# Kernel optimization log

Measured on AMD Instinct MI355X. Metric: run time of the kernel, lower is better.

## Reference

```python
import jax, jax.numpy as jnp
import numpy as np

N = 4096    # channels * n = 4 * 1024
N_IN = 1024
FC = 512


def ldr_layer(x, G, H, subd_A, subd_B, bias):
    """y = W x + bias, where W = sum_i K(A, g_i) K(B, h_i)^T and A, B are
    subdiagonal matrices with entries subd_A, subd_B (Krylov LDR fast multiply).

    Closed form: K(A, g)[i, j] = g[i-j] * c[i] / c[i-j] for i >= j (0 otherwise),
    with c = [1, cumprod(subd_A)]. This turns the multiply into FFT
    correlations/convolutions of length 2n instead of a dense n x n GEMM.
    x: (b, n); G, H: (r, n); subd_A, subd_B: (n-1,); bias: (n,).
    """
    n = x.shape[-1]
    one = jnp.ones((1,), x.dtype)
    c = jnp.concatenate([one, jnp.cumprod(subd_A)])   # (n,) cumulative subdiag products of A
    d = jnp.concatenate([one, jnp.cumprod(subd_B)])   # (n,)
    L = 2 * n
    q = H / d                                          # (r, n)
    gp = G / c                                         # (r, n)
    p = x * d                                          # (b, n)
    # u[b, r, j] = (K(B, h_r)^T x)[j] = sum_k q[r, k] * p[b, j + k]  (cross-correlation)
    Fp = jnp.fft.rfft(p, n=L)                          # (b, n+1)
    Fq = jnp.fft.rfft(q, n=L)                          # (r, n+1)
    u = jnp.fft.irfft(Fp[:, None] * jnp.conj(Fq)[None], n=L)[..., :n]  # (b, r, n)
    # out[b, i] = c[i] * sum_r (gp_r * u[b, r])_conv[i]  (causal convolution)
    Fg = jnp.fft.rfft(gp, n=L)                         # (r, n+1)
    Fu = jnp.fft.rfft(u, n=L)                          # (b, r, n+1)
    out = jnp.fft.irfft(jnp.einsum('rk,brk->bk', Fg, Fu), n=L)[:, :n]
    return c * out + bias


def setup_inputs() -> dict:
    key = jax.random.key(0)
    ks = jax.random.split(key, 14)
    std = 0.01  # params.init_stddev
    f32 = jnp.float32
    inp = {
        'x': jax.random.normal(ks[0], (128, N_IN), f32),
        'G1': std * jax.random.normal(ks[1], (48, N), f32),
        'H1': std * jax.random.normal(ks[2], (48, N), f32),
        'subd_A1': jnp.exp(0.01 * jax.random.normal(ks[3], (N - 1,), f32)),
        'subd_B1': jnp.exp(0.01 * jax.random.normal(ks[4], (N - 1,), f32)),
        'b1': std * jax.random.normal(ks[5], (N,), f32),
        'G2': std * jax.random.normal(ks[6], (16, N), f32),
        'H2': std * jax.random.normal(ks[7], (16, N), f32),
        'subd_A2': jnp.exp(0.01 * jax.random.normal(ks[8], (N - 1,), f32)),
        'subd_B2': jnp.exp(0.01 * jax.random.normal(ks[9], (N - 1,), f32)),
        'b2': std * jax.random.normal(ks[10], (N,), f32),
        'W_logits': jax.random.normal(ks[11], (10, FC), f32) / np.sqrt(FC).astype(np.float32),
        'b_logits': std * jax.random.normal(ks[12], (10,), f32),
    }
    return inp


def reference(x, G1, H1, subd_A1, subd_B1, b1, G2, H2, subd_A2, subd_B2, b2,
              W_logits, b_logits):
    bsz, n_in = x.shape
    xp = jnp.concatenate([x, jnp.zeros((bsz, N - n_in), x.dtype)], axis=-1)  # pad to channels*n
    h = jax.nn.relu(ldr_layer(xp, G1, H1, subd_A1, subd_B1, b1))
    h = jax.nn.relu(ldr_layer(h, G2, H2, subd_A2, subd_B2, b2))
    return h[:, :FC] @ W_logits.T + b_logits
```

## Files before the change

### kernel.cpp

```cpp
#include <hip/hip_runtime.h>
#include <hip/hip_bf16.h>

#define BATCH 128
#define NIN   1024
#define NFULL 4096
#define R1    48
#define R2    16
#define FCDIM 512
#define NOUT  10

#define WS_C1  0
#define WS_D1  4096
#define WS_C2  8192
#define WS_D2  12288
#define WS_Q1  16384
#define WS_GP1 (WS_Q1 + R1*NFULL)
#define WS_Q2  (WS_GP1 + R1*NFULL)
#define WS_GP2 (WS_Q2 + R2*NFULL)
#define WS_P1  (WS_GP2 + R2*NFULL)
#define WS_P2  (WS_P1 + BATCH*NIN)
#define WS_H2  (WS_P2 + BATCH*NFULL)
#define WS_PT1 (WS_H2 + BATCH*FCDIM)
#define WS_P2M (WS_PT1 + NIN*NFULL)
#define WS_CT1 (WS_P2M + FCDIM*NFULL)
#define WS_CT2 (WS_CT1 + 8*5120)
#define WS_VP1 (WS_CT2 + 8*4608)
#define WS_VP2 (WS_VP1 + 4*BATCH*NFULL)
#define WS_END (WS_VP2 + 32*BATCH*FCDIM)

#define NCH 8
#define CH1 (NIN / NCH)
#define CH2 (FCDIM / NCH)
#define CTLD1 5120
#define CTLD2 4608

__global__ void __launch_bounds__(256) prep_fused(
    const float* __restrict__ x, const float* __restrict__ G1,
    const float* __restrict__ H1, const float* __restrict__ G2,
    const float* __restrict__ H2, const float* __restrict__ sA1,
    const float* __restrict__ sB1, const float* __restrict__ sA2,
    const float* __restrict__ sB2, float* __restrict__ ws) {
    __shared__ float cd[4096];
    __shared__ float tot[256];
    int b = blockIdx.x, t = threadIdx.x;
    const float* src;
    int kind, r;
    if (b < 48)       { kind = 0; r = b;       src = sB1; }
    else if (b < 96)  { kind = 1; r = b - 48;  src = sA1; }
    else if (b < 112) { kind = 2; r = b - 96;  src = sB2; }
    else if (b < 128) { kind = 3; r = b - 112; src = sA2; }
    else              { kind = 4; r = b - 128; src = sB1; }
    float loc[16];
    float prod = 1.f;
#pragma unroll
    for (int u = 0; u < 16; ++u) {
        int idx = t * 16 + u;
        float e = (idx == 0) ? 1.f : src[idx - 1];
        prod *= e;
        loc[u] = prod;
    }
    tot[t] = prod;
    __syncthreads();
    for (int off = 1; off < 256; off <<= 1) {
        float v = (t >= off) ? tot[t - off] : 1.f;
        __syncthreads();
        tot[t] *= v;
        __syncthreads();
    }
    float excl = (t == 0) ? 1.f : tot[t - 1];
#pragma unroll
    for (int u = 0; u < 16; ++u) cd[t * 16 + u] = excl * loc[u];
    __syncthreads();

    if (kind == 0) {
        const float* s0 = H1 + (size_t)r * NFULL;
        float* dst = ws + WS_Q1 + (size_t)r * NFULL;
#pragma unroll
        for (int u = 0; u < 16; ++u) { int i = t + u * 256; dst[i] = s0[i] / cd[i]; }
        if (r == 0) { float* d1 = ws + WS_D1;
#pragma unroll
            for (int u = 0; u < 16; ++u) { int i = t + u * 256; d1[i] = cd[i]; } }
    } else if (kind == 1) {
        const float* s0 = G1 + (size_t)r * NFULL;
        float* dst = ws + WS_GP1 + (size_t)r * NFULL;
#pragma unroll
        for (int u = 0; u < 16; ++u) { int i = t + u * 256; dst[i] = s0[i] / cd[i]; }
        if (r == 0) { float* c1 = ws + WS_C1;
#pragma unroll
            for (int u = 0; u < 16; ++u) { int i = t + u * 256; c1[i] = cd[i]; } }
    } else if (kind == 2) {
        const float* s0 = H2 + (size_t)r * NFULL;
        float* dst = ws + WS_Q2 + (size_t)r * NFULL;
#pragma unroll
        for (int u = 0; u < 16; ++u) { int i = t + u * 256; dst[i] = s0[i] / cd[i]; }
        if (r == 0) { float* d2 = ws + WS_D2;
#pragma unroll
            for (int u = 0; u < 16; ++u) { int i = t + u * 256; d2[i] = cd[i]; } }
    } else if (kind == 3) {
        const float* s0 = G2 + (size_t)r * NFULL;
        float* dst = ws + WS_GP2 + (size_t)r * NFULL;
#pragma unroll
        for (int u = 0; u < 16; ++u) { int i = t + u * 256; dst[i] = s0[i] / cd[i]; }
        if (r == 0) { float* c2 = ws + WS_C2;
#pragma unroll
            for (int u = 0; u < 16; ++u) { int i = t + u * 256; c2[i] = cd[i]; } }
    } else {
        int row0 = r * 4;
#pragma unroll
        for (int u = 0; u < 16; ++u) {
            int lin = t + u * 256;
            int row = row0 + (lin >> 10), col = lin & 1023;
            ws[WS_P1 + (size_t)row * NIN + col] = x[(size_t)row * NIN + col] * cd[col];
        }
    }
}

__global__ void gemm_rank_kernel(const float* __restrict__ A, const float* __restrict__ B,
                                 float* __restrict__ C, int Mo, int No, int Kr, int ld) {
    __shared__ float As[48 * 64];
    __shared__ float Bs[48 * 64];
    int tid = threadIdx.x;
    int tx = tid & 15, ty = tid >> 4;
    int n0 = blockIdx.x * 64;
    int m0 = blockIdx.y * 64;
    int tot = Kr * 64;
    for (int lin = tid; lin < tot; lin += 256) {
        int r = lin >> 6, i = lin & 63;
        As[lin] = A[r * ld + m0 + i];
        Bs[lin] = B[r * ld + n0 + i];
    }
    __syncthreads();
    float acc[4][4] = {};
    for (int r = 0; r < Kr; ++r) {
        float a4[4], b4[4];
#pragma unroll
        for (int i = 0; i < 4; ++i) a4[i] = As[r * 64 + ty * 4 + i];
#pragma unroll
        for (int j = 0; j < 4; ++j) b4[j] = Bs[r * 64 + tx * 4 + j];
#pragma unroll
        for (int i = 0; i < 4; ++i)
#pragma unroll
            for (int j = 0; j < 4; ++j) acc[i][j] += a4[i] * b4[j];
    }
#pragma unroll
    for (int i = 0; i < 4; ++i) {
        int m = m0 + ty * 4 + i;
#pragma unroll
        for (int j = 0; j < 4; ++j) {
            C[(size_t)m * No + n0 + tx * 4 + j] = acc[i][j];
        }
    }
}

__global__ void diag_scan_p1(float* __restrict__ ws) {
    const int which = blockIdx.z;
    float* P        = ws + (which == 0 ? WS_PT1 : WS_P2M);
    float* ctot     = ws + (which == 0 ? WS_CT1 : WS_CT2);
    const int R     = which == 0 ? NIN : FCDIM;
    const int CH    = which == 0 ? CH1 : CH2;
    const int nd    = R + NFULL - 1;
    const int ctld  = which == 0 ? CTLD1 : CTLD2;
    int t = blockIdx.x * 256 + threadIdx.x;
    if (t >= nd) return;
    int doff = t - (R - 1);
    int z = blockIdx.y;
    int m0 = z * CH;
    int mlo = max(m0, -doff);
    int mhi = min(m0 + CH, min(NFULL - doff, R));
    float run = 0.f;
    if (mlo < mhi) {
        float* p = P + (size_t)mlo * NFULL + (mlo + doff);
        const size_t step = NFULL + 1;
        int len = mhi - mlo;
        int s = 0;
        for (; s + 8 <= len; s += 8) {
            float v[8];
#pragma unroll
            for (int u = 0; u < 8; ++u) v[u] = p[u * step];
#pragma unroll
            for (int u = 0; u < 8; ++u) { run += v[u]; v[u] = run; }
#pragma unroll
            for (int u = 0; u < 8; ++u) p[u * step] = v[u];
            p += 8 * step;
        }
        for (; s < len; ++s) { float v = *p; run += v; *p = run; p += step; }
    }
    ctot[(size_t)z * ctld + t] = run;
}

__global__ void off_prefix(float* __restrict__ ws) {
    const int which = blockIdx.z;
    float* ct      = ws + (which == 0 ? WS_CT1 : WS_CT2);
    const int ctld = which == 0 ? CTLD1 : CTLD2;
    int t = blockIdx.x * 256 + threadIdx.x;
    if (t >= ctld) return;
    float run = 0.f;
#pragma unroll
    for (int z = 0; z < NCH; ++z) {
        float v = ct[(size_t)z * ctld + t];
        ct[(size_t)z * ctld + t] = run;
        run += v;
    }
}

__global__ void __launch_bounds__(512)
gemm2_l1_kernel(const float* __restrict__ p1, const float* __restrict__ Mt1,
                const float* __restrict__ OFF1, float* __restrict__ vp) {
    __shared__ float As[2][32][68];
    __shared__ float Bs[2][32][68];
    int tid = threadIdx.x;
    int g = tid >> 8;
    int t = tid & 255;
    int tx = t & 15, ty = t >> 4;
    int n0 = blockIdx.x * 64;
    int m0 = blockIdx.y * 64;
    int kbase = blockIdx.z * 256 + g * 128;
    const float* offrow = OFF1 + (size_t)(kbase >> 7) * CTLD1;
    float acc[4][4] = {};
    for (int k0 = kbase; k0 < kbase + 128; k0 += 32) {
#pragma unroll
        for (int l = 0; l < 2; ++l) {
            int lin = t + l * 256;
            int m = lin >> 3, k4 = lin & 7;
            float4 v = *(const float4*)&p1[(size_t)(m0 + m) * NIN + k0 + k4 * 4];
            As[g][k4 * 4 + 0][m] = v.x;
            As[g][k4 * 4 + 1][m] = v.y;
            As[g][k4 * 4 + 2][m] = v.z;
            As[g][k4 * 4 + 3][m] = v.w;
        }
#pragma unroll
        for (int l = 0; l < 2; ++l) {
            int lin = t + l * 256;
            int k = lin >> 4, n4 = lin & 15;
            float4 v = *(const float4*)&Mt1[(size_t)(k0 + k) * NFULL + n0 + n4 * 4];
            const float* o = &offrow[1023 + n0 + n4 * 4 - (k0 + k)];
            v.x += o[0]; v.y += o[1]; v.z += o[2]; v.w += o[3];
            *(float4*)&Bs[g][k][n4 * 4] = v;
        }
        __syncthreads();
#pragma unroll
        for (int kk = 0; kk < 32; ++kk) {
            float4 a4 = *(const float4*)&As[g][kk][ty * 4];
            float4 b4 = *(const float4*)&Bs[g][kk][tx * 4];
            acc[0][0] += a4.x * b4.x; acc[0][1] += a4.x * b4.y;
            acc[0][2] += a4.x * b4.z; acc[0][3] += a4.x * b4.w;
            acc[1][0] += a4.y * b4.x; acc[1][1] += a4.y * b4.y;
            acc[1][2] += a4.y * b4.z; acc[1][3] += a4.y * b4.w;
            acc[2][0] += a4.z * b4.x; acc[2][1] += a4.z * b4.y;
            acc[2][2] += a4.z * b4.z; acc[2][3] += a4.z * b4.w;
            acc[3][0] += a4.w * b4.x; acc[3][1] += a4.w * b4.y;
            acc[3][2] += a4.w * b4.z; acc[3][3] += a4.w * b4.w;
        }
        __syncthreads();
    }
    float* red = &As[0][0][0];
    if (g == 1) {
#pragma unroll
        for (int i = 0; i < 4; ++i)
            *(float4*)&red[(ty * 4 + i) * 64 + tx * 4] =
                make_float4(acc[i][0], acc[i][1], acc[i][2], acc[i][3]);
    }
    __syncthreads();
    if (g == 0) {
        float* dst = vp + (size_t)blockIdx.z * BATCH * NFULL;
#pragma unroll
        for (int i = 0; i < 4; ++i) {
            int m = m0 + ty * 4 + i;
            float4 r = *(const float4*)&red[(ty * 4 + i) * 64 + tx * 4];
            *(float4*)&dst[(size_t)m * NFULL + n0 + tx * 4] =
                make_float4(acc[i][0] + r.x, acc[i][1] + r.y,
                            acc[i][2] + r.z, acc[i][3] + r.w);
        }
    }
}

__global__ void reduce_l1_kernel(const float* __restrict__ vp, const float* __restrict__ c1,
                                 const float* __restrict__ b1, const float* __restrict__ d2,
                                 float* __restrict__ p2) {
    int idx4 = blockIdx.x * 256 + threadIdx.x;
    int base = idx4 * 4;
    int n = base & (NFULL - 1);
    float4 s = make_float4(0.f, 0.f, 0.f, 0.f);
#pragma unroll
    for (int z = 0; z < 4; ++z) {
        float4 v = *(const float4*)&vp[(size_t)z * BATCH * NFULL + base];
        s.x += v.x; s.y += v.y; s.z += v.z; s.w += v.w;
    }
    float4 cc = *(const float4*)&c1[n];
    float4 bb = *(const float4*)&b1[n];
    float4 dd = *(const float4*)&d2[n];
    float4 o;
    o.x = fmaxf(cc.x * s.x + bb.x, 0.f) * dd.x;
    o.y = fmaxf(cc.y * s.y + bb.y, 0.f) * dd.y;
    o.z = fmaxf(cc.z * s.z + bb.z, 0.f) * dd.z;
    o.w = fmaxf(cc.w * s.w + bb.w, 0.f) * dd.w;
    *(float4*)&p2[base] = o;
}

__global__ void gemm2_l2_kernel(const float* __restrict__ p2, const float* __restrict__ M2,
                                const float* __restrict__ OFF2, float* __restrict__ vp) {
    __shared__ float As[32][68];
    __shared__ float Bs[32][68];
    int t = threadIdx.x;
    int tx = t & 15, ty = t >> 4;
    int n0 = blockIdx.x * 64;
    int m0 = blockIdx.y * 64;
    int kbase = blockIdx.z * 128;
    const float* offrow = OFF2 + (size_t)(n0 >> 6) * CTLD2;
    float acc[4][4] = {};
    for (int k0 = kbase; k0 < kbase + 128; k0 += 32) {
#pragma unroll
        for (int l = 0; l < 2; ++l) {
            int lin = t + l * 256;
            int m = lin >> 3, k4 = lin & 7;
            float4 v = *(const float4*)&p2[(size_t)(m0 + m) * NFULL + k0 + k4 * 4];
            As[k4 * 4 + 0][m] = v.x;
            As[k4 * 4 + 1][m] = v.y;
            As[k4 * 4 + 2][m] = v.z;
            As[k4 * 4 + 3][m] = v.w;
        }
#pragma unroll
        for (int l = 0; l < 2; ++l) {
            int lin = t + l * 256;
            int n = lin >> 3, k4 = lin & 7;
            float4 v = *(const float4*)&M2[(size_t)(n0 + n) * NFULL + k0 + k4 * 4];
            const float* o = &offrow[511 + k0 + k4 * 4 - (n0 + n)];
            v.x += o[0]; v.y += o[1]; v.z += o[2]; v.w += o[3];
            Bs[k4 * 4 + 0][n] = v.x;
            Bs[k4 * 4 + 1][n] = v.y;
            Bs[k4 * 4 + 2][n] = v.z;
            Bs[k4 * 4 + 3][n] = v.w;
        }
        __syncthreads();
#pragma unroll
        for (int kk = 0; kk < 32; ++kk) {
            float4 a4 = *(const float4*)&As[kk][ty * 4];
            float4 b4 = *(const float4*)&Bs[kk][tx * 4];
            acc[0][0] += a4.x * b4.x; acc[0][1] += a4.x * b4.y;
            acc[0][2] += a4.x * b4.z; acc[0][3] += a4.x * b4.w;
            acc[1][0] += a4.y * b4.x; acc[1][1] += a4.y * b4.y;
            acc[1][2] += a4.y * b4.z; acc[1][3] += a4.y * b4.w;
            acc[2][0] += a4.z * b4.x; acc[2][1] += a4.z * b4.y;
            acc[2][2] += a4.z * b4.z; acc[2][3] += a4.z * b4.w;
            acc[3][0] += a4.w * b4.x; acc[3][1] += a4.w * b4.y;
            acc[3][2] += a4.w * b4.z; acc[3][3] += a4.w * b4.w;
        }
        __syncthreads();
    }
#pragma unroll
    for (int i = 0; i < 4; ++i) {
        int m = m0 + ty * 4 + i;
        *(float4*)&vp[((size_t)blockIdx.z * BATCH + m) * FCDIM + n0 + tx * 4] =
            make_float4(acc[i][0], acc[i][1], acc[i][2], acc[i][3]);
    }
}

__global__ void fused_out_kernel(const float* __restrict__ vp, const float* __restrict__ c2,
                                 const float* __restrict__ b2, const float* __restrict__ Wl,
                                 const float* __restrict__ bl, float* __restrict__ out) {
    __shared__ float h2s[FCDIM];
    int b = blockIdx.x, t = threadIdx.x;
    for (int col = t; col < FCDIM; col += 256) {
        float s = 0.f;
#pragma unroll
        for (int z = 0; z < 32; ++z)
            s += vp[((size_t)z * BATCH + b) * FCDIM + col];
        h2s[col] = fmaxf(c2[col] * s + b2[col], 0.f);
    }
    __syncthreads();
    int w = t >> 6, lane = t & 63;
    for (int o = w; o < NOUT; o += 4) {
        float s = 0.f;
#pragma unroll
        for (int i = lane; i < FCDIM; i += 64) s += h2s[i] * Wl[(size_t)o * FCDIM + i];
#pragma unroll
        for (int off = 32; off > 0; off >>= 1) s += __shfl_down(s, off);
        if (lane == 0) out[(size_t)b * NOUT + o] = s + bl[o];
    }
}

extern "C" void kernel_launch(void* const* d_in, const int* in_sizes, int n_in,
                              void* d_out, int out_size, void* d_ws, size_t ws_size,
                              hipStream_t stream) {
    const float* x   = (const float*)d_in[0];
    const float* G1  = (const float*)d_in[1];
    const float* H1  = (const float*)d_in[2];
    const float* sA1 = (const float*)d_in[3];
    const float* sB1 = (const float*)d_in[4];
    const float* b1  = (const float*)d_in[5];
    const float* G2  = (const float*)d_in[6];
    const float* H2  = (const float*)d_in[7];
    const float* sA2 = (const float*)d_in[8];
    const float* sB2 = (const float*)d_in[9];
    const float* b2  = (const float*)d_in[10];
    const float* Wl  = (const float*)d_in[11];
    const float* bl  = (const float*)d_in[12];
    float* out = (float*)d_out;
    float* ws = (float*)d_ws;
    (void)in_sizes; (void)n_in; (void)out_size; (void)ws_size;

    prep_fused<<<160, 256, 0, stream>>>(x, G1, H1, G2, H2, sA1, sB1, sA2, sB2, ws);

    gemm_rank_kernel<<<dim3(64, 16), 256, 0, stream>>>(ws + WS_Q1, ws + WS_GP1, ws + WS_PT1,
                                                       NIN, NFULL, R1, NFULL);
    gemm_rank_kernel<<<dim3(64, 8), 256, 0, stream>>>(ws + WS_GP2, ws + WS_Q2, ws + WS_P2M,
                                                      FCDIM, NFULL, R2, NFULL);

    diag_scan_p1<<<dim3(20, NCH, 2), 256, 0, stream>>>(ws);
    off_prefix<<<dim3(20, 1, 2), 256, 0, stream>>>(ws);

    gemm2_l1_kernel<<<dim3(64, 2, 4), 512, 0, stream>>>(ws + WS_P1, ws + WS_PT1,
                                                        ws + WS_CT1, ws + WS_VP1);
    reduce_l1_kernel<<<512, 256, 0, stream>>>(ws + WS_VP1, ws + WS_C1, b1, ws + WS_D2,
                                              ws + WS_P2);

    gemm2_l2_kernel<<<dim3(8, 2, 32), 256, 0, stream>>>(ws + WS_P2, ws + WS_P2M,
                                                        ws + WS_CT2, ws + WS_VP2);

    fused_out_kernel<<<BATCH, 256, 0, stream>>>(ws + WS_VP2, ws + WS_C2, b2, Wl, bl, out);
}
```

Before: 86.11 us.

## Widen batch tiles in gemm2 kernels, merge rank GEMMs, finer diagonal scan chunks

The two low-rank outer-product GEMMs become a single launch that uses a z index, float4 shared-memory loads and stores, and padded shared tiles. The diagonal prefix scan for layer 1 now uses 16 chunks of 64 rows instead of 8, with the inner unroll raised to 16, and the offset table layout is changed to match. Both gemm2 kernels now cover all 128 batch rows in one block, using 1024 or 512 threads, so the Toeplitz-corrected B tile is loaded and offset-added once per block instead of twice. The cost is fewer, larger blocks, higher register and LDS pressure, and more chunk totals to prefix-sum.

```diff
diff --git a/kernel.cpp b/kernel.cpp
--- a/kernel.cpp
+++ b/kernel.cpp
@@ -23,14 +23,14 @@
 #define WS_PT1 (WS_H2 + BATCH*FCDIM)
 #define WS_P2M (WS_PT1 + NIN*NFULL)
 #define WS_CT1 (WS_P2M + FCDIM*NFULL)
-#define WS_CT2 (WS_CT1 + 8*5120)
+#define WS_CT2 (WS_CT1 + 16*5120)
 #define WS_VP1 (WS_CT2 + 8*4608)
 #define WS_VP2 (WS_VP1 + 4*BATCH*NFULL)
 #define WS_END (WS_VP2 + 32*BATCH*FCDIM)
 
-#define NCH 8
-#define CH1 (NIN / NCH)
-#define CH2 (FCDIM / NCH)
+#define NCH1 16
+#define NCH2 8
+#define CHROWS 64
 #define CTLD1 5120
 #define CTLD2 4608
 
@@ -115,73 +115,79 @@
     }
 }
 
-__global__ void gemm_rank_kernel(const float* __restrict__ A, const float* __restrict__ B,
-                                 float* __restrict__ C, int Mo, int No, int Kr, int ld) {
-    __shared__ float As[48 * 64];
-    __shared__ float Bs[48 * 64];
+__global__ void __launch_bounds__(256) gemm_rank_kernel(float* __restrict__ ws) {
+    const int which = blockIdx.z;
+    if (which == 1 && blockIdx.y >= 8) return;
+    const float* A = ws + (which == 0 ? WS_Q1  : WS_GP2);
+    const float* B = ws + (which == 0 ? WS_GP1 : WS_Q2);
+    float* C       = ws + (which == 0 ? WS_PT1 : WS_P2M);
+    const int Kr   = which == 0 ? R1 : R2;
+    __shared__ float As[R1 * 68];
+    __shared__ float Bs[R1 * 68];
     int tid = threadIdx.x;
     int tx = tid & 15, ty = tid >> 4;
     int n0 = blockIdx.x * 64;
     int m0 = blockIdx.y * 64;
-    int tot = Kr * 64;
-    for (int lin = tid; lin < tot; lin += 256) {
-        int r = lin >> 6, i = lin & 63;
-        As[lin] = A[r * ld + m0 + i];
-        Bs[lin] = B[r * ld + n0 + i];
+    int nf4 = Kr * 16;
+    for (int lin = tid; lin < nf4; lin += 256) {
+        int r = lin >> 4, i4 = lin & 15;
+        *(float4*)&As[r * 68 + i4 * 4] = *(const float4*)&A[(size_t)r * NFULL + m0 + i4 * 4];
+        *(float4*)&Bs[r * 68 + i4 * 4] = *(const float4*)&B[(size_t)r * NFULL + n0 + i4 * 4];
     }
     __syncthreads();
     float acc[4][4] = {};
+#pragma unroll 8
     for (int r = 0; r < Kr; ++r) {
-        float a4[4], b4[4];
-#pragma unroll
-        for (int i = 0; i < 4; ++i) a4[i] = As[r * 64 + ty * 4 + i];
-#pragma unroll
-        for (int j = 0; j < 4; ++j) b4[j] = Bs[r * 64 + tx * 4 + j];
-#pragma unroll
-        for (int i = 0; i < 4; ++i)
-#pragma unroll
-            for (int j = 0; j < 4; ++j) acc[i][j] += a4[i] * b4[j];
+        float4 a4 = *(const float4*)&As[r * 68 + ty * 4];
+        float4 b4 = *(const float4*)&Bs[r * 68 + tx * 4];
+        acc[0][0] += a4.x * b4.x; acc[0][1] += a4.x * b4.y;
+        acc[0][2] += a4.x * b4.z; acc[0][3] += a4.x * b4.w;
+        acc[1][0] += a4.y * b4.x; acc[1][1] += a4.y * b4.y;
+        acc[1][2] += a4.y * b4.z; acc[1][3] += a4.y * b4.w;
+        acc[2][0] += a4.z * b4.x; acc[2][1] += a4.z * b4.y;
+        acc[2][2] += a4.z * b4.z; acc[2][3] += a4.z * b4.w;
+        acc[3][0] += a4.w * b4.x; acc[3][1] += a4.w * b4.y;
+        acc[3][2] += a4.w * b4.z; acc[3][3] += a4.w * b4.w;
     }
 #pragma unroll
     for (int i = 0; i < 4; ++i) {
         int m = m0 + ty * 4 + i;
-#pragma unroll
-        for (int j = 0; j < 4; ++j) {
-            C[(size_t)m * No + n0 + tx * 4 + j] = acc[i][j];
-        }
+        *(float4*)&C[(size_t)m * NFULL + n0 + tx * 4] =
+            make_float4(acc[i][0], acc[i][1], acc[i][2], acc[i][3]);
     }
 }
 
 __global__ void diag_scan_p1(float* __restrict__ ws) {
     const int which = blockIdx.z;
+    const int nch   = which == 0 ? NCH1 : NCH2;
+    if (blockIdx.y >= (unsigned)nch) return;
     float* P        = ws + (which == 0 ? WS_PT1 : WS_P2M);
     float* ctot     = ws + (which == 0 ? WS_CT1 : WS_CT2);
     const int R     = which == 0 ? NIN : FCDIM;
-    const int CH    = which == 0 ? CH1 : CH2;
     const int nd    = R + NFULL - 1;
     const int ctld  = which == 0 ? CTLD1 : CTLD2;
     int t = blockIdx.x * 256 + threadIdx.x;
     if (t >= nd) return;
     int doff = t - (R - 1);
     int z = blockIdx.y;
-    int m0 = z * CH;
+    int m0 = z * CHROWS;
     int mlo = max(m0, -doff);
-    int mhi = min(m0 + CH, min(NFULL - doff, R));
+    int mhi = min(m0 + CHROWS, min(NFULL - doff, R));
     float run = 0.f;
     if (mlo < mhi) {
         float* p = P + (size_t)mlo * NFULL + (mlo + doff);
         const size_t step = NFULL + 1;
         int len = mhi - mlo;
         int s = 0;
-        for (; s + 8 <= len; s += 8) {
-            float v[8];
-#pragma unroll
-            for (int u = 0; u < 8; ++u) v[u] = p[u * step];
-#pragma unroll
-            for (int u = 0; u < 8; ++u) { run += v[u]; v[u] = run; }
-#pragma unroll
-            for (int u = 0; u < 8; ++u) p[u * step] = v[u];
-            p += 8 * step;
+        for (; s + 16 <= len; s += 16) {
+            float v[16];
+#pragma unroll
+            for (int u = 0; u < 16; ++u) v[u] = p[u * step];
+#pragma unroll
+            for (int u = 0; u < 16; ++u) { run += v[u]; v[u] = run; }
+#pragma unroll
+            for (int u = 0; u < 16; ++u) p[u * step] = v[u];
+            p += 16 * step;
         }
         for (; s < len; ++s) { float v = *p; run += v; *p = run; p += step; }
     }
@@ -192,48 +198,45 @@
     const int which = blockIdx.z;
     float* ct      = ws + (which == 0 ? WS_CT1 : WS_CT2);
     const int ctld = which == 0 ? CTLD1 : CTLD2;
+    const int nch  = which == 0 ? NCH1 : NCH2;
     int t = blockIdx.x * 256 + threadIdx.x;
     if (t >= ctld) return;
     float run = 0.f;
-#pragma unroll
-    for (int z = 0; z < NCH; ++z) {
+    for (int z = 0; z < nch; ++z) {
         float v = ct[(size_t)z * ctld + t];
         ct[(size_t)z * ctld + t] = run;
         run += v;
     }
 }
 
-__global__ void __launch_bounds__(512)
+__global__ void __launch_bounds__(1024)
 gemm2_l1_kernel(const float* __restrict__ p1, const float* __restrict__ Mt1,
                 const float* __restrict__ OFF1, float* __restrict__ vp) {
-    __shared__ float As[2][32][68];
+    __shared__ float As[2][32][132];
     __shared__ float Bs[2][32][68];
     int tid = threadIdx.x;
-    int g = tid >> 8;
-    int t = tid & 255;
+    int g = tid >> 9;
+    int t = tid & 511;
     int tx = t & 15, ty = t >> 4;
     int n0 = blockIdx.x * 64;
-    int m0 = blockIdx.y * 64;
     int kbase = blockIdx.z * 256 + g * 128;
-    const float* offrow = OFF1 + (size_t)(kbase >> 7) * CTLD1;
     float acc[4][4] = {};
     for (int k0 = kbase; k0 < kbase + 128; k0 += 32) {
+        const float* orow = OFF1 + (size_t)(k0 >> 6) * CTLD1;
 #pragma unroll
         for (int l = 0; l < 2; ++l) {
-            int lin = t + l * 256;
+            int lin = t + l * 512;
             int m = lin >> 3, k4 = lin & 7;
-            float4 v = *(const float4*)&p1[(size_t)(m0 + m) * NIN + k0 + k4 * 4];
+            float4 v = *(const float4*)&p1[(size_t)m * NIN + k0 + k4 * 4];
             As[g][k4 * 4 + 0][m] = v.x;
             As[g][k4 * 4 + 1][m] = v.y;
             As[g][k4 * 4 + 2][m] = v.z;
             As[g][k4 * 4 + 3][m] = v.w;
         }
-#pragma unroll
-        for (int l = 0; l < 2; ++l) {
-            int lin = t + l * 256;
-            int k = lin >> 4, n4 = lin & 15;
+        {
+            int k = t >> 4, n4 = t & 15;
             float4 v = *(const float4*)&Mt1[(size_t)(k0 + k) * NFULL + n0 + n4 * 4];
-            const float* o = &offrow[1023 + n0 + n4 * 4 - (k0 + k)];
+            const float* o = &orow[1023 + n0 + n4 * 4 - (k0 + k)];
             v.x += o[0]; v.y += o[1]; v.z += o[2]; v.w += o[3];
             *(float4*)&Bs[g][k][n4 * 4] = v;
         }
@@ -265,8 +268,8 @@
         float* dst = vp + (size_t)blockIdx.z * BATCH * NFULL;
 #pragma unroll
         for (int i = 0; i < 4; ++i) {
-            int m = m0 + ty * 4 + i;
-            float4 r = *(const float4*)&red[(ty * 4 + i) * 64 + tx * 4];
+            int m = ty * 4 + i;
+            float4 r = *(const float4*)&red[m * 64 + tx * 4];
             *(float4*)&dst[(size_t)m * NFULL + n0 + tx * 4] =
                 make_float4(acc[i][0] + r.x, acc[i][1] + r.y,
                             acc[i][2] + r.z, acc[i][3] + r.w);
@@ -297,32 +300,30 @@
     *(float4*)&p2[base] = o;
 }
 
-__global__ void gemm2_l2_kernel(const float* __restrict__ p2, const float* __restrict__ M2,
-                                const float* __restrict__ OFF2, float* __restrict__ vp) {
-    __shared__ float As[32][68];
+__global__ void __launch_bounds__(512)
+gemm2_l2_kernel(const float* __restrict__ p2, const float* __restrict__ M2,
+                const float* __restrict__ OFF2, float* __restrict__ vp) {
+    __shared__ float As[32][132];
     __shared__ float Bs[32][68];
     int t = threadIdx.x;
     int tx = t & 15, ty = t >> 4;
     int n0 = blockIdx.x * 64;
-    int m0 = blockIdx.y * 64;
     int kbase = blockIdx.z * 128;
     const float* offrow = OFF2 + (size_t)(n0 >> 6) * CTLD2;
     float acc[4][4] = {};
     for (int k0 = kbase; k0 < kbase + 128; k0 += 32) {
 #pragma unroll
         for (int l = 0; l < 2; ++l) {
-            int lin = t + l * 256;
+            int lin = t + l * 512;
             int m = lin >> 3, k4 = lin & 7;
-            float4 v = *(const float4*)&p2[(size_t)(m0 + m) * NFULL + k0 + k4 * 4];
+            float4 v = *(const float4*)&p2[(size_t)m * NFULL + k0 + k4 * 4];
             As[k4 * 4 + 0][m] = v.x;
             As[k4 * 4 + 1][m] = v.y;
             As[k4 * 4 + 2][m] = v.z;
             As[k4 * 4 + 3][m] = v.w;
         }
-#pragma unroll
-        for (int l = 0; l < 2; ++l) {
-            int lin = t + l * 256;
-            int n = lin >> 3, k4 = lin & 7;
+        {
+            int n = t >> 3, k4 = t & 7;
             float4 v = *(const float4*)&M2[(size_t)(n0 + n) * NFULL + k0 + k4 * 4];
             const float* o = &offrow[511 + k0 + k4 * 4 - (n0 + n)];
             v.x += o[0]; v.y += o[1]; v.z += o[2]; v.w += o[3];
@@ -349,7 +350,7 @@
     }
 #pragma unroll
     for (int i = 0; i < 4; ++i) {
-        int m = m0 + ty * 4 + i;
+        int m = ty * 4 + i;
         *(float4*)&vp[((size_t)blockIdx.z * BATCH + m) * FCDIM + n0 + tx * 4] =
             make_float4(acc[i][0], acc[i][1], acc[i][2], acc[i][3]);
     }
@@ -401,20 +402,17 @@
 
     prep_fused<<<160, 256, 0, stream>>>(x, G1, H1, G2, H2, sA1, sB1, sA2, sB2, ws);
 
-    gemm_rank_kernel<<<dim3(64, 16), 256, 0, stream>>>(ws + WS_Q1, ws + WS_GP1, ws + WS_PT1,
-                                                       NIN, NFULL, R1, NFULL);
-    gemm_rank_kernel<<<dim3(64, 8), 256, 0, stream>>>(ws + WS_GP2, ws + WS_Q2, ws + WS_P2M,
-                                                      FCDIM, NFULL, R2, NFULL);
-
-    diag_scan_p1<<<dim3(20, NCH, 2), 256, 0, stream>>>(ws);
+    gemm_rank_kernel<<<dim3(64, 16, 2), 256, 0, stream>>>(ws);
+
+    diag_scan_p1<<<dim3(20, NCH1, 2), 256, 0, stream>>>(ws);
     off_prefix<<<dim3(20, 1, 2), 256, 0, stream>>>(ws);
 
-    gemm2_l1_kernel<<<dim3(64, 2, 4), 512, 0, stream>>>(ws + WS_P1, ws + WS_PT1,
-                                                        ws + WS_CT1, ws + WS_VP1);
+    gemm2_l1_kernel<<<dim3(64, 1, 4), 1024, 0, stream>>>(ws + WS_P1, ws + WS_PT1,
+                                                         ws + WS_CT1, ws + WS_VP1);
     reduce_l1_kernel<<<512, 256, 0, stream>>>(ws + WS_VP1, ws + WS_C1, b1, ws + WS_D2,
                                               ws + WS_P2);
 
-    gemm2_l2_kernel<<<dim3(8, 2, 32), 256, 0, stream>>>(ws + WS_P2, ws + WS_P2M,
+    gemm2_l2_kernel<<<dim3(8, 1, 32), 512, 0, stream>>>(ws + WS_P2, ws + WS_P2M,
                                                         ws + WS_CT2, ws + WS_VP2);
 
     fused_out_kernel<<<BATCH, 256, 0, stream>>>(ws + WS_VP2, ws + WS_C2, b2, Wl, bl, out);
```

New measurement: 79.89 us. 1.08x faster.
